# Kernel tuning notes

Hardware: AMD Instinct MI355X
Metric: run time of the kernel (lower is better)

The kernel has to match this reference:

```python
import jax, jax.numpy as jnp
import numpy as np

D_MODEL = 1024
NUM_HEADS = 16
DEPTH = D_MODEL // NUM_HEADS
B, S = 2, 2048


def setup_inputs() -> dict:
    key = jax.random.key(0)
    ks = jax.random.split(key, 11)
    scale = 1.0 / np.sqrt(D_MODEL)
    inp = {
        "v": jax.random.normal(ks[0], (B, S, D_MODEL), dtype=jnp.float32),
        "k": jax.random.normal(ks[1], (B, S, D_MODEL), dtype=jnp.float32),
        "q": jax.random.normal(ks[2], (B, S, D_MODEL), dtype=jnp.float32),
        "wq": jax.random.normal(ks[3], (D_MODEL, D_MODEL), dtype=jnp.float32) * scale,
        "bq": jnp.zeros((D_MODEL,), dtype=jnp.float32),
        "wk": jax.random.normal(ks[4], (D_MODEL, D_MODEL), dtype=jnp.float32) * scale,
        "bk": jnp.zeros((D_MODEL,), dtype=jnp.float32),
        "wv": jax.random.normal(ks[5], (D_MODEL, D_MODEL), dtype=jnp.float32) * scale,
        "bv": jnp.zeros((D_MODEL,), dtype=jnp.float32),
        "wo": jax.random.normal(ks[6], (D_MODEL, D_MODEL), dtype=jnp.float32) * scale,
        "bo": jnp.zeros((D_MODEL,), dtype=jnp.float32),
    }
    return inp


def _split_heads(x):
    # (B, S, D) -> (B, H, S, depth)
    b, s, _ = x.shape
    return x.reshape(b, s, NUM_HEADS, DEPTH).transpose(0, 2, 1, 3)


def reference(v, k, q, wq, bq, wk, bk, wv, bv, wo, bo):
    qh = _split_heads(q @ wq + bq)  # (B,H,S,d)
    kh = _split_heads(k @ wk + bk)
    vh = _split_heads(v @ wv + bv)
    scores = jnp.einsum("bhqd,bhkd->bhqk", qh, kh) / jnp.sqrt(
        jnp.asarray(DEPTH, dtype=qh.dtype))
    attn = jax.nn.softmax(scores, axis=-1)
    out = jnp.einsum("bhqk,bhkd->bhqd", attn, vh)  # (B,H,S,d)
    out = out.transpose(0, 2, 1, 3).reshape(q.shape[0], -1, D_MODEL)
    return out @ wo + bo
```

## Files before the change

kernel.cpp:

```cpp
#include <hip/hip_runtime.h>
#include <hip/hip_bf16.h>

#define S_LEN 2048
#define DM 1024
#define NH 16
#define DH 64
#define MROWS 4096

typedef __hip_bfloat16 hbf;
typedef __attribute__((ext_vector_type(4))) float floatx4;
typedef __bf16 bf16x8 __attribute__((ext_vector_type(8)));

#define QSCALE 0.18033688f
#define EXP_BIAS 5.77078016f

__device__ __forceinline__ void gload_lds16(const void* g, void* l) {
  __builtin_amdgcn_global_load_lds(
      (const __attribute__((address_space(1))) unsigned int*)g,
      (__attribute__((address_space(3))) unsigned int*)l, 16, 0, 0);
}

__global__ __launch_bounds__(256) void cvt3w(
    const float* __restrict__ q, const float* __restrict__ k, const float* __restrict__ v,
    hbf* __restrict__ Xq, hbf* __restrict__ Xk, hbf* __restrict__ Xv,
    const float* __restrict__ wq, const float* __restrict__ wk,
    const float* __restrict__ wv, const float* __restrict__ wo,
    hbf* __restrict__ Wqt, hbf* __restrict__ Wkt,
    hbf* __restrict__ Wvt, hbf* __restrict__ Wot) {
  __shared__ float tile[64][65];
  if (blockIdx.y < 3) {
    const float* src; hbf* dst;
    switch (blockIdx.y) {
      case 0:  src = q; dst = Xq; break;
      case 1:  src = k; dst = Xk; break;
      default: src = v; dst = Xv; break;
    }
    int i = blockIdx.x * 256 + threadIdx.x;
    float4 val = ((const float4*)src)[i];
    union { hbf h[4]; uint2 u; } pk;
    pk.h[0] = __float2bfloat16(val.x);
    pk.h[1] = __float2bfloat16(val.y);
    pk.h[2] = __float2bfloat16(val.z);
    pk.h[3] = __float2bfloat16(val.w);
    ((uint2*)dst)[i] = pk.u;
    return;
  }
  if (blockIdx.x >= 1024) return;
  const float* W; hbf* Wt;
  switch (blockIdx.x >> 8) {
    case 0:  W = wq; Wt = Wqt; break;
    case 1:  W = wk; Wt = Wkt; break;
    case 2:  W = wv; Wt = Wvt; break;
    default: W = wo; Wt = Wot; break;
  }
  const int t8 = blockIdx.x & 255;
  const int n0 = (t8 & 15) * 64, k0 = (t8 >> 4) * 64;
  const int t = threadIdx.x;
  const int col = t & 63, rb = t >> 6;
#pragma unroll
  for (int i = 0; i < 16; ++i) {
    int row = i * 4 + rb;
    tile[row][col] = W[(size_t)(k0 + row) * DM + n0 + col];
  }
  __syncthreads();
#pragma unroll
  for (int i = 0; i < 16; ++i) {
    int row = i * 4 + rb;
    Wt[(size_t)(n0 + row) * DM + k0 + col] = __float2bfloat16(tile[col][row]);
  }
}

__global__ __launch_bounds__(256) void gemm_qkv(
    const hbf* __restrict__ Xq, const hbf* __restrict__ Xk, const hbf* __restrict__ Xv,
    const hbf* __restrict__ Wqt, const hbf* __restrict__ Wkt, const hbf* __restrict__ Wvt,
    const float* __restrict__ bq, const float* __restrict__ bk, const float* __restrict__ bv,
    hbf* __restrict__ Qh, hbf* __restrict__ Kf, hbf* __restrict__ Vf) {
  const hbf* A; const hbf* Wt; const float* bias; hbf* Out; float oscale;
  const int z = blockIdx.z;
  if (z == 0)      { A = Xq; Wt = Wqt; bias = bq; Out = Qh; oscale = QSCALE; }
  else if (z == 1) { A = Xk; Wt = Wkt; bias = bk; Out = Kf; oscale = 1.0f; }
  else             { A = Xv; Wt = Wvt; bias = bv; Out = Vf; oscale = 1.0f; }

  __shared__ __align__(16) hbf As[128 * 32];
  __shared__ __align__(16) hbf Bs[128 * 32];

  const int tid = threadIdx.x;
  const int lane = tid & 63, wave = tid >> 6;
  const int l15 = lane & 15, quad = lane >> 4;
  const int wm = wave >> 1, wn = wave & 1;
  const int m0 = blockIdx.x * 128, n0 = blockIdx.y * 128;

  floatx4 acc[4][4] = {};

#pragma unroll 1
  for (int k0 = 0; k0 < DM; k0 += 32) {
#pragma unroll
    for (int it = 0; it < 2; ++it) {
      int c = tid + it * 256;
      int row = c >> 2, cc = (c & 3) << 3;
      gload_lds16(&A[(size_t)(m0 + row) * DM + k0 + cc], &As[row * 32 + cc]);
      gload_lds16(&Wt[(size_t)(n0 + row) * DM + k0 + cc], &Bs[row * 32 + cc]);
    }
    __syncthreads();
    bf16x8 af[4], bfr[4];
#pragma unroll
    for (int mi = 0; mi < 4; ++mi)
      af[mi] = *(const bf16x8*)&As[(wm * 64 + mi * 16 + l15) * 32 + quad * 8];
#pragma unroll
    for (int ni = 0; ni < 4; ++ni)
      bfr[ni] = *(const bf16x8*)&Bs[(wn * 64 + ni * 16 + l15) * 32 + quad * 8];
#pragma unroll
    for (int mi = 0; mi < 4; ++mi)
#pragma unroll
      for (int ni = 0; ni < 4; ++ni)
        acc[mi][ni] = __builtin_amdgcn_mfma_f32_16x16x32_bf16(af[mi], bfr[ni], acc[mi][ni], 0, 0, 0);
    __syncthreads();
  }

#pragma unroll
  for (int mi = 0; mi < 4; ++mi) {
#pragma unroll
    for (int ni = 0; ni < 4; ++ni) {
      int col = n0 + wn * 64 + ni * 16 + l15;
      float bb_ = bias[col];
#pragma unroll
      for (int r = 0; r < 4; ++r) {
        int row = m0 + wm * 64 + mi * 16 + quad * 4 + r;
        float vv = (acc[mi][ni][r] + bb_) * oscale;
        int b = row >> 11, s = row & 2047, h = col >> 6, dd = col & 63;
        int bh = b * NH + h;
        size_t idx;
        if (z == 1) {
          int kt = s >> 5, nif = (s >> 4) & 1, fl15 = s & 15;
          int ksf = dd >> 5, fquad = (dd >> 3) & 3, e = dd & 7;
          idx = (((size_t)bh * 64 + kt) * 4 + ksf * 2 + nif) * 512 + (fquad * 16 + fl15) * 8 + e;
        } else if (z == 2) {
          int kt = s >> 5, fquad = (s >> 3) & 3, e = s & 7;
          int nd = dd >> 4, fl15 = dd & 15;
          idx = (((size_t)bh * 64 + kt) * 4 + nd) * 512 + (fquad * 16 + fl15) * 8 + e;
        } else {
          idx = (((size_t)bh * S_LEN + s) << 6) + dd;
        }
        Out[idx] = __float2bfloat16(vv);
      }
    }
  }
}

__global__ __launch_bounds__(256, 4) void flash_attn(
    const hbf* __restrict__ Qh, const hbf* __restrict__ Kf,
    const hbf* __restrict__ Vf, hbf* __restrict__ AO) {
  const int id = blockIdx.x;
  const int bh = (id & 7) * 4 + (id >> 8);
  const int q0 = ((id >> 3) & 31) * 64;
  const int b = bh >> 4, h = bh & 15;
  const int tid = threadIdx.x;
  const int lane = tid & 63, wave = tid >> 6;
  const int qw = wave & 1;
  const int ksplit = wave >> 1;
  const int l15 = lane & 15, quad = lane >> 4;

  __shared__ __align__(16) unsigned char smem[17408];
  __shared__ float Lbuf[2][32];
  hbf* Pw = (hbf*)(smem + wave * 2560);

  const size_t qbase = (((size_t)bh) * S_LEN + q0 + qw * 32) * DH;
  bf16x8 qf[2][2];
#pragma unroll
  for (int mi = 0; mi < 2; ++mi)
#pragma unroll
    for (int ks = 0; ks < 2; ++ks)
      qf[mi][ks] = *(const bf16x8*)&Qh[qbase + (size_t)(mi * 16 + l15) * DH + ks * 32 + quad * 8];

  bf16x8 ones_f;
  {
    const __bf16 ov = (l15 == 0) ? (__bf16)1.0f : (__bf16)0.0f;
#pragma unroll
    for (int j = 0; j < 8; ++j) ones_f[j] = ov;
  }

  floatx4 o[2][4] = {};
  floatx4 lsum[2] = {};

  const hbf* Kb = Kf + ((size_t)bh * 64 + ksplit * 32) * 2048 + lane * 8;
  const hbf* Vb = Vf + ((size_t)bh * 64 + ksplit * 32) * 2048 + lane * 8;

  bf16x8 kf[2][2], vf[4];
#pragma unroll
  for (int ni = 0; ni < 2; ++ni)
#pragma unroll
    for (int ks = 0; ks < 2; ++ks)
      kf[ni][ks] = *(const bf16x8*)&Kb[(ks * 2 + ni) * 512];
#pragma unroll
  for (int nd = 0; nd < 4; ++nd)
    vf[nd] = *(const bf16x8*)&Vb[nd * 512];

#pragma unroll 1
  for (int it = 0; it < 32; ++it) {
    const int tn = (it == 31) ? 0 : (it + 1) * 2048;

    floatx4 sacc[2][2] = {};
#pragma unroll
    for (int ks = 0; ks < 2; ++ks)
#pragma unroll
      for (int mi = 0; mi < 2; ++mi)
#pragma unroll
        for (int ni = 0; ni < 2; ++ni)
          sacc[mi][ni] = __builtin_amdgcn_mfma_f32_16x16x32_bf16(qf[mi][ks], kf[ni][ks], sacc[mi][ni], 0, 0, 0);

#pragma unroll
    for (int ni = 0; ni < 2; ++ni)
#pragma unroll
      for (int ks = 0; ks < 2; ++ks)
        kf[ni][ks] = *(const bf16x8*)&Kb[tn + (ks * 2 + ni) * 512];

#pragma unroll
    for (int mi = 0; mi < 2; ++mi)
#pragma unroll
      for (int ni = 0; ni < 2; ++ni)
#pragma unroll
        for (int r = 0; r < 4; ++r) {
          float p = exp2f(sacc[mi][ni][r] - EXP_BIAS);
          Pw[(mi * 16 + quad * 4 + r) * 40 + ni * 16 + l15] = __float2bfloat16(p);
        }

    bf16x8 pf[2];
#pragma unroll
    for (int mi = 0; mi < 2; ++mi)
      pf[mi] = *(const bf16x8*)&Pw[(mi * 16 + l15) * 40 + quad * 8];

#pragma unroll
    for (int mi = 0; mi < 2; ++mi)
      lsum[mi] = __builtin_amdgcn_mfma_f32_16x16x32_bf16(pf[mi], ones_f, lsum[mi], 0, 0, 0);

#pragma unroll
    for (int nd = 0; nd < 4; ++nd)
#pragma unroll
      for (int mi = 0; mi < 2; ++mi)
        o[mi][nd] = __builtin_amdgcn_mfma_f32_16x16x32_bf16(pf[mi], vf[nd], o[mi][nd], 0, 0, 0);

#pragma unroll
    for (int nd = 0; nd < 4; ++nd)
      vf[nd] = *(const bf16x8*)&Vb[tn + nd * 512];
  }

  __syncthreads();
  if (ksplit == 1) {
    float* Ob = (float*)smem + qw * (32 * 68);
#pragma unroll
    for (int mi = 0; mi < 2; ++mi)
#pragma unroll
      for (int nd = 0; nd < 4; ++nd)
#pragma unroll
        for (int r = 0; r < 4; ++r)
          Ob[(mi * 16 + quad * 4 + r) * 68 + nd * 16 + l15] = o[mi][nd][r];
    if (l15 == 0) {
#pragma unroll
      for (int mi = 0; mi < 2; ++mi)
#pragma unroll
        for (int r = 0; r < 4; ++r)
          Lbuf[qw][mi * 16 + quad * 4 + r] = lsum[mi][r];
    }
  }
  __syncthreads();
  if (ksplit == 0) {
    const float* Ob = (const float*)smem + qw * (32 * 68);
#pragma unroll
    for (int mi = 0; mi < 2; ++mi) {
      float linv[4];
#pragma unroll
      for (int r = 0; r < 4; ++r) {
        float lq = __shfl(lsum[mi][r], lane & 48, 64) + Lbuf[qw][mi * 16 + quad * 4 + r];
        linv[r] = 1.0f / lq;
      }
#pragma unroll
      for (int nd = 0; nd < 4; ++nd) {
#pragma unroll
        for (int r = 0; r < 4; ++r) {
          int rl = mi * 16 + quad * 4 + r;
          int qrow = q0 + qw * 32 + rl;
          int dd = nd * 16 + l15;
          float vv = (o[mi][nd][r] + Ob[rl * 68 + dd]) * linv[r];
          AO[(((size_t)b * S_LEN + qrow) << 10) + h * DH + dd] = __float2bfloat16(vv);
        }
      }
    }
  }
}

__global__ __launch_bounds__(256) void gemm_out(
    const hbf* __restrict__ A, const hbf* __restrict__ Wt,
    const float* __restrict__ bias, float* __restrict__ Out) {
  __shared__ __align__(16) hbf As[128 * 32];
  __shared__ __align__(16) hbf Bs[64 * 32];

  const int tid = threadIdx.x;
  const int lane = tid & 63, wave = tid >> 6;
  const int l15 = lane & 15, quad = lane >> 4;
  const int wm = wave >> 1, wn = wave & 1;
  const int m0 = blockIdx.x * 128, n0 = blockIdx.y * 64;

  floatx4 acc[4][2] = {};

#pragma unroll 1
  for (int k0 = 0; k0 < DM; k0 += 32) {
#pragma unroll
    for (int it = 0; it < 2; ++it) {
      int c = tid + it * 256;
      int row = c >> 2, cc = (c & 3) << 3;
      gload_lds16(&A[(size_t)(m0 + row) * DM + k0 + cc], &As[row * 32 + cc]);
    }
    {
      int row = tid >> 2, cc = (tid & 3) << 3;
      gload_lds16(&Wt[(size_t)(n0 + row) * DM + k0 + cc], &Bs[row * 32 + cc]);
    }
    __syncthreads();
    bf16x8 af[4], bfr[2];
#pragma unroll
    for (int mi = 0; mi < 4; ++mi)
      af[mi] = *(const bf16x8*)&As[(wm * 64 + mi * 16 + l15) * 32 + quad * 8];
#pragma unroll
    for (int ni = 0; ni < 2; ++ni)
      bfr[ni] = *(const bf16x8*)&Bs[(wn * 32 + ni * 16 + l15) * 32 + quad * 8];
#pragma unroll
    for (int mi = 0; mi < 4; ++mi)
#pragma unroll
      for (int ni = 0; ni < 2; ++ni)
        acc[mi][ni] = __builtin_amdgcn_mfma_f32_16x16x32_bf16(af[mi], bfr[ni], acc[mi][ni], 0, 0, 0);
    __syncthreads();
  }

#pragma unroll
  for (int mi = 0; mi < 4; ++mi) {
#pragma unroll
    for (int ni = 0; ni < 2; ++ni) {
      int col = n0 + wn * 32 + ni * 16 + l15;
      float bb_ = bias[col];
#pragma unroll
      for (int r = 0; r < 4; ++r) {
        int row = m0 + wm * 64 + mi * 16 + quad * 4 + r;
        Out[(size_t)row * DM + col] = acc[mi][ni][r] + bb_;
      }
    }
  }
}

extern "C" void kernel_launch(void* const* d_in, const int* in_sizes, int n_in,
                              void* d_out, int out_size, void* d_ws, size_t ws_size,
                              hipStream_t stream) {
  const float* v  = (const float*)d_in[0];
  const float* k  = (const float*)d_in[1];
  const float* q  = (const float*)d_in[2];
  const float* wq = (const float*)d_in[3];
  const float* bq = (const float*)d_in[4];
  const float* wk = (const float*)d_in[5];
  const float* bk = (const float*)d_in[6];
  const float* wv = (const float*)d_in[7];
  const float* bv = (const float*)d_in[8];
  const float* wo = (const float*)d_in[9];
  const float* bo = (const float*)d_in[10];

  const size_t NX = (size_t)MROWS * DM;
  const size_t NW = (size_t)DM * DM;
  hbf* base = (hbf*)d_ws;
  hbf* Xq  = base;
  hbf* Xk  = Xq + NX;
  hbf* Xv  = Xk + NX;
  hbf* Wqt = Xv + NX;
  hbf* Wkt = Wqt + NW;
  hbf* Wvt = Wkt + NW;
  hbf* Wot = Wvt + NW;
  hbf* Qh  = Wot + NW;
  hbf* Kf  = Qh + NX;
  hbf* Vf  = Kf + NX;
  hbf* AO  = Vf + NX;

  cvt3w<<<dim3(4096, 4), 256, 0, stream>>>(q, k, v, Xq, Xk, Xv,
                                           wq, wk, wv, wo, Wqt, Wkt, Wvt, Wot);
  gemm_qkv<<<dim3(32, 8, 3), 256, 0, stream>>>(Xq, Xk, Xv, Wqt, Wkt, Wvt, bq, bk, bv, Qh, Kf, Vf);
  flash_attn<<<1024, 256, 0, stream>>>(Qh, Kf, Vf, AO);
  gemm_out<<<dim3(32, 16), 256, 0, stream>>>(AO, Wot, bo, (float*)d_out);
}
```

Before: 254.5 us.

## Pre-swizzle GEMM operands into MFMA fragment layout and drop LDS staging

```diff
diff --git a/kernel.cpp b/kernel.cpp
--- a/kernel.cpp
+++ b/kernel.cpp
@@ -14,48 +14,55 @@
 #define QSCALE 0.18033688f
 #define EXP_BIAS 5.77078016f
 
-__device__ __forceinline__ void gload_lds16(const void* g, void* l) {
-  __builtin_amdgcn_global_load_lds(
-      (const __attribute__((address_space(1))) unsigned int*)g,
-      (__attribute__((address_space(3))) unsigned int*)l, 16, 0, 0);
-}
 
 __global__ __launch_bounds__(256) void cvt3w(
     const float* __restrict__ q, const float* __restrict__ k, const float* __restrict__ v,
-    hbf* __restrict__ Xq, hbf* __restrict__ Xk, hbf* __restrict__ Xv,
+    hbf* __restrict__ Xqh, hbf* __restrict__ Xkh, hbf* __restrict__ Xvh,
     const float* __restrict__ wq, const float* __restrict__ wk,
     const float* __restrict__ wv, const float* __restrict__ wo,
-    hbf* __restrict__ Wqt, hbf* __restrict__ Wkt,
-    hbf* __restrict__ Wvt, hbf* __restrict__ Wot) {
+    hbf* __restrict__ Wqh, hbf* __restrict__ Wkh,
+    hbf* __restrict__ Wvh, hbf* __restrict__ Woh) {
   __shared__ float tile[64][65];
+  const int t = threadIdx.x;
   if (blockIdx.y < 3) {
     const float* src; hbf* dst;
     switch (blockIdx.y) {
-      case 0:  src = q; dst = Xq; break;
-      case 1:  src = k; dst = Xk; break;
-      default: src = v; dst = Xv; break;
-    }
-    int i = blockIdx.x * 256 + threadIdx.x;
-    float4 val = ((const float4*)src)[i];
-    union { hbf h[4]; uint2 u; } pk;
-    pk.h[0] = __float2bfloat16(val.x);
-    pk.h[1] = __float2bfloat16(val.y);
-    pk.h[2] = __float2bfloat16(val.z);
-    pk.h[3] = __float2bfloat16(val.w);
-    ((uint2*)dst)[i] = pk.u;
+      case 0:  src = q; dst = Xqh; break;
+      case 1:  src = k; dst = Xkh; break;
+      default: src = v; dst = Xvh; break;
+    }
+    const int mt = blockIdx.x >> 4, kt = blockIdx.x & 15;
+    const int s0 = mt * 64, k0 = kt * 64;
+    const int col = t & 63, rb = t >> 6;
+#pragma unroll
+    for (int i = 0; i < 16; ++i) {
+      int row = i * 4 + rb;
+      tile[row][col] = src[(size_t)(s0 + row) * DM + k0 + col];
+    }
+    __syncthreads();
+    const int lanep = t & 63, l15p = lanep & 15, quadp = lanep >> 4;
+#pragma unroll
+    for (int it = 0; it < 2; ++it) {
+      int fl = (t >> 6) * 2 + it;
+      int fm = fl >> 1, fk = fl & 1;
+      union { hbf h[8]; uint4 u; } pk;
+#pragma unroll
+      for (int j = 0; j < 8; ++j)
+        pk.h[j] = __float2bfloat16(tile[fm * 16 + l15p][fk * 32 + quadp * 8 + j]);
+      size_t base = ((size_t)(mt * 4 + fm) * 32 + (kt * 2 + fk)) * 512 + lanep * 8;
+      *(uint4*)&dst[base] = pk.u;
+    }
     return;
   }
-  if (blockIdx.x >= 1024) return;
-  const float* W; hbf* Wt;
+  const float* W; hbf* Wh;
   switch (blockIdx.x >> 8) {
-    case 0:  W = wq; Wt = Wqt; break;
-    case 1:  W = wk; Wt = Wkt; break;
-    case 2:  W = wv; Wt = Wvt; break;
-    default: W = wo; Wt = Wot; break;
+    case 0:  W = wq; Wh = Wqh; break;
+    case 1:  W = wk; Wh = Wkh; break;
+    case 2:  W = wv; Wh = Wvh; break;
+    default: W = wo; Wh = Woh; break;
   }
   const int t8 = blockIdx.x & 255;
   const int n0 = (t8 & 15) * 64, k0 = (t8 >> 4) * 64;
-  const int t = threadIdx.x;
   const int col = t & 63, rb = t >> 6;
 #pragma unroll
   for (int i = 0; i < 16; ++i) {
@@ -65,83 +72,96 @@
   __syncthreads();
 #pragma unroll
   for (int i = 0; i < 16; ++i) {
-    int row = i * 4 + rb;
-    Wt[(size_t)(n0 + row) * DM + k0 + col] = __float2bfloat16(tile[col][row]);
+    int rowi = i * 4 + rb;
+    int nn = n0 + rowi, kk = k0 + col;
+    size_t idx = ((size_t)(nn >> 4) * 32 + (kk >> 5)) * 512 +
+                 ((((kk >> 3) & 3) * 16 + (nn & 15)) * 8) + (kk & 7);
+    Wh[idx] = __float2bfloat16(tile[col][rowi]);
   }
 }
 
 __global__ __launch_bounds__(256) void gemm_qkv(
-    const hbf* __restrict__ Xq, const hbf* __restrict__ Xk, const hbf* __restrict__ Xv,
-    const hbf* __restrict__ Wqt, const hbf* __restrict__ Wkt, const hbf* __restrict__ Wvt,
+    const hbf* __restrict__ Xqh, const hbf* __restrict__ Xkh, const hbf* __restrict__ Xvh,
+    const hbf* __restrict__ Wqh, const hbf* __restrict__ Wkh, const hbf* __restrict__ Wvh,
     const float* __restrict__ bq, const float* __restrict__ bk, const float* __restrict__ bv,
     hbf* __restrict__ Qh, hbf* __restrict__ Kf, hbf* __restrict__ Vf) {
-  const hbf* A; const hbf* Wt; const float* bias; hbf* Out; float oscale;
-  const int z = blockIdx.z;
-  if (z == 0)      { A = Xq; Wt = Wqt; bias = bq; Out = Qh; oscale = QSCALE; }
-  else if (z == 1) { A = Xk; Wt = Wkt; bias = bk; Out = Kf; oscale = 1.0f; }
-  else             { A = Xv; Wt = Wvt; bias = bv; Out = Vf; oscale = 1.0f; }
-
-  __shared__ __align__(16) hbf As[128 * 32];
-  __shared__ __align__(16) hbf Bs[128 * 32];
+  const int id = blockIdx.x;
+  const int x = id & 7, idx = id >> 3;
+  const int z = idx >> 5, rem = idx & 31;
+  const int nblk = rem >> 1, mblk = rem & 1;
+
+  const hbf* Ah; const hbf* Bh; const float* bias; hbf* Out; float oscale;
+  if (z == 0)      { Ah = Xqh; Bh = Wqh; bias = bq; Out = Qh; oscale = QSCALE; }
+  else if (z == 1) { Ah = Xkh; Bh = Wkh; bias = bk; Out = Kf; oscale = 1.0f; }
+  else             { Ah = Xvh; Bh = Wvh; bias = bv; Out = Vf; oscale = 1.0f; }
 
   const int tid = threadIdx.x;
   const int lane = tid & 63, wave = tid >> 6;
   const int l15 = lane & 15, quad = lane >> 4;
-  const int wm = wave >> 1, wn = wave & 1;
-  const int m0 = blockIdx.x * 128, n0 = blockIdx.y * 128;
+  const int M0 = x * 512 + mblk * 256 + wave * 64;
+  const int n0 = nblk * 64;
+
+  const hbf* ap = Ah + (size_t)(M0 >> 4) * 32 * 512 + lane * 8;
+  const hbf* bp = Bh + (size_t)(n0 >> 4) * 32 * 512 + lane * 8;
 
   floatx4 acc[4][4] = {};
+  bf16x8 a0[4], b0[4], a1[4], b1[4];
+#pragma unroll
+  for (int i = 0; i < 4; ++i) {
+    a0[i] = *(const bf16x8*)&ap[(size_t)i * 16384];
+    b0[i] = *(const bf16x8*)&bp[(size_t)i * 16384];
+  }
 
 #pragma unroll 1
-  for (int k0 = 0; k0 < DM; k0 += 32) {
-#pragma unroll
-    for (int it = 0; it < 2; ++it) {
-      int c = tid + it * 256;
-      int row = c >> 2, cc = (c & 3) << 3;
-      gload_lds16(&A[(size_t)(m0 + row) * DM + k0 + cc], &As[row * 32 + cc]);
-      gload_lds16(&Wt[(size_t)(n0 + row) * DM + k0 + cc], &Bs[row * 32 + cc]);
-    }
-    __syncthreads();
-    bf16x8 af[4], bfr[4];
+  for (int kb = 0; kb < 32; kb += 2) {
+#pragma unroll
+    for (int i = 0; i < 4; ++i) {
+      a1[i] = *(const bf16x8*)&ap[(size_t)i * 16384 + (kb + 1) * 512];
+      b1[i] = *(const bf16x8*)&bp[(size_t)i * 16384 + (kb + 1) * 512];
+    }
 #pragma unroll
     for (int mi = 0; mi < 4; ++mi)
-      af[mi] = *(const bf16x8*)&As[(wm * 64 + mi * 16 + l15) * 32 + quad * 8];
-#pragma unroll
-    for (int ni = 0; ni < 4; ++ni)
-      bfr[ni] = *(const bf16x8*)&Bs[(wn * 64 + ni * 16 + l15) * 32 + quad * 8];
+#pragma unroll
+      for (int ni = 0; ni < 4; ++ni)
+        acc[mi][ni] = __builtin_amdgcn_mfma_f32_16x16x32_bf16(a0[mi], b0[ni], acc[mi][ni], 0, 0, 0);
+    const int k2 = (kb + 2) & 31;
+#pragma unroll
+    for (int i = 0; i < 4; ++i) {
+      a0[i] = *(const bf16x8*)&ap[(size_t)i * 16384 + k2 * 512];
+      b0[i] = *(const bf16x8*)&bp[(size_t)i * 16384 + k2 * 512];
+    }
 #pragma unroll
     for (int mi = 0; mi < 4; ++mi)
 #pragma unroll
       for (int ni = 0; ni < 4; ++ni)
-        acc[mi][ni] = __builtin_amdgcn_mfma_f32_16x16x32_bf16(af[mi], bfr[ni], acc[mi][ni], 0, 0, 0);
-    __syncthreads();
+        acc[mi][ni] = __builtin_amdgcn_mfma_f32_16x16x32_bf16(a1[mi], b1[ni], acc[mi][ni], 0, 0, 0);
   }
 
 #pragma unroll
   for (int mi = 0; mi < 4; ++mi) {
 #pragma unroll
     for (int ni = 0; ni < 4; ++ni) {
-      int col = n0 + wn * 64 + ni * 16 + l15;
+      int col = n0 + ni * 16 + l15;
       float bb_ = bias[col];
 #pragma unroll
       for (int r = 0; r < 4; ++r) {
-        int row = m0 + wm * 64 + mi * 16 + quad * 4 + r;
+        int row = M0 + mi * 16 + quad * 4 + r;
         float vv = (acc[mi][ni][r] + bb_) * oscale;
         int b = row >> 11, s = row & 2047, h = col >> 6, dd = col & 63;
         int bh = b * NH + h;
-        size_t idx;
+        size_t idxo;
         if (z == 1) {
           int kt = s >> 5, nif = (s >> 4) & 1, fl15 = s & 15;
           int ksf = dd >> 5, fquad = (dd >> 3) & 3, e = dd & 7;
-          idx = (((size_t)bh * 64 + kt) * 4 + ksf * 2 + nif) * 512 + (fquad * 16 + fl15) * 8 + e;
+          idxo = (((size_t)bh * 64 + kt) * 4 + ksf * 2 + nif) * 512 + (fquad * 16 + fl15) * 8 + e;
         } else if (z == 2) {
           int kt = s >> 5, fquad = (s >> 3) & 3, e = s & 7;
           int nd = dd >> 4, fl15 = dd & 15;
-          idx = (((size_t)bh * 64 + kt) * 4 + nd) * 512 + (fquad * 16 + fl15) * 8 + e;
+          idxo = (((size_t)bh * 64 + kt) * 4 + nd) * 512 + (fquad * 16 + fl15) * 8 + e;
         } else {
-          idx = (((size_t)bh * S_LEN + s) << 6) + dd;
+          idxo = (((size_t)bh * S_LEN + s) << 6) + dd;
         }
-        Out[idx] = __float2bfloat16(vv);
+        Out[idxo] = __float2bfloat16(vv);
       }
     }
   }
@@ -273,15 +293,18 @@
         float lq = __shfl(lsum[mi][r], lane & 48, 64) + Lbuf[qw][mi * 16 + quad * 4 + r];
         linv[r] = 1.0f / lq;
       }
+      const int m16 = (b * S_LEN + q0 + qw * 32 + mi * 16) >> 4;
 #pragma unroll
       for (int nd = 0; nd < 4; ++nd) {
+        const int kb = h * 2 + (nd >> 1);
+        const int qa = ((nd & 1) << 1) + (l15 >> 3);
+        const int dd = nd * 16 + l15;
 #pragma unroll
         for (int r = 0; r < 4; ++r) {
           int rl = mi * 16 + quad * 4 + r;
-          int qrow = q0 + qw * 32 + rl;
-          int dd = nd * 16 + l15;
           float vv = (o[mi][nd][r] + Ob[rl * 68 + dd]) * linv[r];
-          AO[(((size_t)b * S_LEN + qrow) << 10) + h * DH + dd] = __float2bfloat16(vv);
+          size_t idxo = ((size_t)m16 * 32 + kb) * 512 + (qa * 16 + quad * 4 + r) * 8 + (l15 & 7);
+          AO[idxo] = __float2bfloat16(vv);
         }
       }
     }
@@ -289,56 +312,60 @@
 }
 
 __global__ __launch_bounds__(256) void gemm_out(
-    const hbf* __restrict__ A, const hbf* __restrict__ Wt,
+    const hbf* __restrict__ Ah, const hbf* __restrict__ Bh,
     const float* __restrict__ bias, float* __restrict__ Out) {
-  __shared__ __align__(16) hbf As[128 * 32];
-  __shared__ __align__(16) hbf Bs[64 * 32];
-
+  const int id = blockIdx.x;
+  const int x = id & 7, idx = id >> 3;
+  const int nblk = idx >> 3, mblk = idx & 7;
   const int tid = threadIdx.x;
   const int lane = tid & 63, wave = tid >> 6;
   const int l15 = lane & 15, quad = lane >> 4;
   const int wm = wave >> 1, wn = wave & 1;
-  const int m0 = blockIdx.x * 128, n0 = blockIdx.y * 64;
-
-  floatx4 acc[4][2] = {};
+  const int M0 = x * 512 + mblk * 64 + wm * 32;
+  const int n0 = nblk * 128 + wn * 64;
+
+  const hbf* ap = Ah + (size_t)(M0 >> 4) * 32 * 512 + lane * 8;
+  const hbf* bp = Bh + (size_t)(n0 >> 4) * 32 * 512 + lane * 8;
+
+  floatx4 acc[2][4] = {};
+  bf16x8 a0[2], b0[4], a1[2], b1[4];
+#pragma unroll
+  for (int i = 0; i < 2; ++i) a0[i] = *(const bf16x8*)&ap[(size_t)i * 16384];
+#pragma unroll
+  for (int i = 0; i < 4; ++i) b0[i] = *(const bf16x8*)&bp[(size_t)i * 16384];
 
 #pragma unroll 1
-  for (int k0 = 0; k0 < DM; k0 += 32) {
-#pragma unroll
-    for (int it = 0; it < 2; ++it) {
-      int c = tid + it * 256;
-      int row = c >> 2, cc = (c & 3) << 3;
-      gload_lds16(&A[(size_t)(m0 + row) * DM + k0 + cc], &As[row * 32 + cc]);
-    }
-    {
-      int row = tid >> 2, cc = (tid & 3) << 3;
-      gload_lds16(&Wt[(size_t)(n0 + row) * DM + k0 + cc], &Bs[row * 32 + cc]);
-    }
-    __syncthreads();
-    bf16x8 af[4], bfr[2];
-#pragma unroll
-    for (int mi = 0; mi < 4; ++mi)
-      af[mi] = *(const bf16x8*)&As[(wm * 64 + mi * 16 + l15) * 32 + quad * 8];
-#pragma unroll
-    for (int ni = 0; ni < 2; ++ni)
-      bfr[ni] = *(const bf16x8*)&Bs[(wn * 32 + ni * 16 + l15) * 32 + quad * 8];
-#pragma unroll
-    for (int mi = 0; mi < 4; ++mi)
-#pragma unroll
-      for (int ni = 0; ni < 2; ++ni)
-        acc[mi][ni] = __builtin_amdgcn_mfma_f32_16x16x32_bf16(af[mi], bfr[ni], acc[mi][ni], 0, 0, 0);
-    __syncthreads();
-  }
-
-#pragma unroll
-  for (int mi = 0; mi < 4; ++mi) {
-#pragma unroll
-    for (int ni = 0; ni < 2; ++ni) {
-      int col = n0 + wn * 32 + ni * 16 + l15;
+  for (int kb = 0; kb < 32; kb += 2) {
+#pragma unroll
+    for (int i = 0; i < 2; ++i) a1[i] = *(const bf16x8*)&ap[(size_t)i * 16384 + (kb + 1) * 512];
+#pragma unroll
+    for (int i = 0; i < 4; ++i) b1[i] = *(const bf16x8*)&bp[(size_t)i * 16384 + (kb + 1) * 512];
+#pragma unroll
+    for (int mi = 0; mi < 2; ++mi)
+#pragma unroll
+      for (int ni = 0; ni < 4; ++ni)
+        acc[mi][ni] = __builtin_amdgcn_mfma_f32_16x16x32_bf16(a0[mi], b0[ni], acc[mi][ni], 0, 0, 0);
+    const int k2 = (kb + 2) & 31;
+#pragma unroll
+    for (int i = 0; i < 2; ++i) a0[i] = *(const bf16x8*)&ap[(size_t)i * 16384 + k2 * 512];
+#pragma unroll
+    for (int i = 0; i < 4; ++i) b0[i] = *(const bf16x8*)&bp[(size_t)i * 16384 + k2 * 512];
+#pragma unroll
+    for (int mi = 0; mi < 2; ++mi)
+#pragma unroll
+      for (int ni = 0; ni < 4; ++ni)
+        acc[mi][ni] = __builtin_amdgcn_mfma_f32_16x16x32_bf16(a1[mi], b1[ni], acc[mi][ni], 0, 0, 0);
+  }
+
+#pragma unroll
+  for (int mi = 0; mi < 2; ++mi) {
+#pragma unroll
+    for (int ni = 0; ni < 4; ++ni) {
+      int col = n0 + ni * 16 + l15;
       float bb_ = bias[col];
 #pragma unroll
       for (int r = 0; r < 4; ++r) {
-        int row = m0 + wm * 64 + mi * 16 + quad * 4 + r;
+        int row = M0 + mi * 16 + quad * 4 + r;
         Out[(size_t)row * DM + col] = acc[mi][ni][r] + bb_;
       }
     }
@@ -363,21 +390,21 @@
   const size_t NX = (size_t)MROWS * DM;
   const size_t NW = (size_t)DM * DM;
   hbf* base = (hbf*)d_ws;
-  hbf* Xq  = base;
-  hbf* Xk  = Xq + NX;
-  hbf* Xv  = Xk + NX;
-  hbf* Wqt = Xv + NX;
-  hbf* Wkt = Wqt + NW;
-  hbf* Wvt = Wkt + NW;
-  hbf* Wot = Wvt + NW;
-  hbf* Qh  = Wot + NW;
+  hbf* Xqh = base;
+  hbf* Xkh = Xqh + NX;
+  hbf* Xvh = Xkh + NX;
+  hbf* Wqh = Xvh + NX;
+  hbf* Wkh = Wqh + NW;
+  hbf* Wvh = Wkh + NW;
+  hbf* Woh = Wvh + NW;
+  hbf* Qh  = Woh + NW;
   hbf* Kf  = Qh + NX;
   hbf* Vf  = Kf + NX;
-  hbf* AO  = Vf + NX;
-
-  cvt3w<<<dim3(4096, 4), 256, 0, stream>>>(q, k, v, Xq, Xk, Xv,
-                                           wq, wk, wv, wo, Wqt, Wkt, Wvt, Wot);
-  gemm_qkv<<<dim3(32, 8, 3), 256, 0, stream>>>(Xq, Xk, Xv, Wqt, Wkt, Wvt, bq, bk, bv, Qh, Kf, Vf);
-  flash_attn<<<1024, 256, 0, stream>>>(Qh, Kf, Vf, AO);
-  gemm_out<<<dim3(32, 16), 256, 0, stream>>>(AO, Wot, bo, (float*)d_out);
+  hbf* AOh = Vf + NX;
+
+  cvt3w<<<dim3(1024, 4), 256, 0, stream>>>(q, k, v, Xqh, Xkh, Xvh,
+                                           wq, wk, wv, wo, Wqh, Wkh, Wvh, Woh);
+  gemm_qkv<<<768, 256, 0, stream>>>(Xqh, Xkh, Xvh, Wqh, Wkh, Wvh, bq, bk, bv, Qh, Kf, Vf);
+  flash_attn<<<1024, 256, 0, stream>>>(Qh, Kf, Vf, AOh);
+  gemm_out<<<512, 256, 0, stream>>>(AOh, Woh, bo, (float*)d_out);
 }
```

Result: faster. 242.2 us (-4.8%).
